# Optimization experiments

Measured on AMD Instinct MI355X. Metric: run time of the kernel, lower is better.

The kernel has to match this reference:

```python
import jax, jax.numpy as jnp
import numpy as np

B, S, D = 8, 1024, 1024          # batch, sentence_len, instance_size
H = 16                            # n_head
HEAD_SIZE = 1024                  # Head_size (== D here)
HD = HEAD_SIZE // H               # multi_head_size = 64


def setup_inputs() -> dict:
    key = jax.random.key(0)
    k1, k2, k3 = jax.random.split(key, 3)
    x = jax.random.normal(k1, (B, S, D), dtype=jnp.float32)
    padding_mask = jnp.ones((B, 1, S), dtype=jnp.float32)  # 1 = valid key token
    # nn.Linear(instance_size, 3*Head_size, bias=False): store as [D, 3*HEAD_SIZE]
    Wqkv = jax.random.normal(k2, (D, 3 * HEAD_SIZE), dtype=jnp.float32) / np.sqrt(D)
    # nn.Linear(Head_size, instance_size): weight [HEAD_SIZE, D] + bias [D]
    Wproj = jax.random.normal(k3, (HEAD_SIZE, D), dtype=jnp.float32) / np.sqrt(HEAD_SIZE)
    bproj = jnp.zeros((D,), dtype=jnp.float32)
    return {"x": x, "padding_mask": padding_mask, "Wqkv": Wqkv, "Wproj": Wproj, "bproj": bproj}


def reference(x, padding_mask, Wqkv, Wproj, bproj):
    Bn, Sn, _ = x.shape
    qkv = x @ Wqkv                                  # [B,S,3*HEAD_SIZE]
    q, k, v = jnp.split(qkv, 3, axis=2)
    # [B,S,H,hd] -> [B,H,S,hd]
    q = q.reshape(Bn, Sn, H, HD).transpose(0, 2, 1, 3)
    k = k.reshape(Bn, Sn, H, HD).transpose(0, 2, 1, 3)
    v = v.reshape(Bn, Sn, H, HD).transpose(0, 2, 1, 3)
    # scores [B,H,S,S]
    scores = jnp.einsum('bhqd,bhkd->bhqk', q, k) / np.sqrt(HD)
    # padding_mask [B,1,S] -> additive bias over key dim, broadcast over heads/queries
    mask_w = -(1.0 - padding_mask) * 1e10          # [B,1,S]
    scores = scores + mask_w[:, None]              # [B,1,1,S] broadcast
    probas = jax.nn.softmax(scores, axis=-1)
    probas = probas * padding_mask[:, None]        # zero out padded keys (as in torch code)
    # dropout p=0 (eval) -> identity
    out = jnp.einsum('bhqk,bhkd->bhqd', probas, v)  # [B,H,S,hd]
    out = out.transpose(0, 2, 1, 3).reshape(Bn, Sn, HEAD_SIZE)
    return out @ Wproj + bproj
```

## Files before the change

kernel.cpp:

```cpp
#include <hip/hip_runtime.h>
#include <stdint.h>

typedef short s16x8 __attribute__((ext_vector_type(8)));
typedef float f32x4 __attribute__((ext_vector_type(4)));
typedef unsigned short u16;
typedef unsigned short u16x4 __attribute__((ext_vector_type(4)));
typedef unsigned int u32x2 __attribute__((ext_vector_type(2)));

#define B_ 8
#define S_ 1024
#define C1 0.18033688f
#define KADV ((size_t)64 * 3072)

__device__ __forceinline__ u16 f2bf(float f) {
  union { float f; unsigned u; } v; v.f = f;
  unsigned u = v.u;
  unsigned r = (u + 0x7FFFu + ((u >> 16) & 1u)) >> 16;
  return (u16)r;
}

__device__ __forceinline__ void gll16(const u16* src, u16* dst) {
  __builtin_amdgcn_global_load_lds((const __attribute__((address_space(1))) void*)src,
                                   (__attribute__((address_space(3))) void*)dst, 16, 0, 0);
}

__global__ void k_cvt(const float* __restrict__ in, u16* __restrict__ out, int n4) {
  int i = blockIdx.x * blockDim.x + threadIdx.x;
  int stride = gridDim.x * blockDim.x;
  for (; i < n4; i += stride) {
    float4 v = ((const float4*)in)[i];
    u16x4 o;
    o.x = f2bf(v.x); o.y = f2bf(v.y); o.z = f2bf(v.z); o.w = f2bf(v.w);
    ((u16x4*)out)[i] = o;
  }
}

__global__ void k_mbias(const float* __restrict__ m, float* __restrict__ mb, int n) {
  int i = blockIdx.x * blockDim.x + threadIdx.x;
  if (i < n) mb[i] = (m[i] - 1.f) * 1.443e10f;
}

__global__ void k_tpose(const float* __restrict__ in, u16* __restrict__ out, int R, int C) {
  __shared__ float tile[64][65];
  int c0 = blockIdx.x * 64, r0 = blockIdx.y * 64;
  int t = threadIdx.x;
#pragma unroll
  for (int it = 0; it < 16; ++it) {
    int r = it * 4 + (t >> 6), c = t & 63;
    tile[r][c] = in[(size_t)(r0 + r) * C + c0 + c];
  }
  __syncthreads();
#pragma unroll
  for (int it = 0; it < 16; ++it) {
    int c = it * 4 + (t >> 6), r = t & 63;
    out[(size_t)(c0 + c) * R + r0 + r] = f2bf(tile[r][c]);
  }
}

template<int ROWS>
__device__ __forceinline__ void stage_swz(const u16* __restrict__ g, size_t goff, size_t ld,
                                          u16* lds, int wave, int lane) {
#pragma unroll
  for (int c = 0; c < ROWS / 32; ++c) {
    int jb = (wave * (ROWS / 32) + c) * 64;
    int j = jb + lane;
    int row = j >> 3;
    int s = (j & 7) ^ (row & 7);
    const u16* src = g + goff + (size_t)row * ld + s * 8;
    u16* dst = lds + jb * 8;
    gll16(src, dst);
  }
}

__device__ __forceinline__ s16x8 frag_read(const u16* lds, int row, int slotk) {
  int s = slotk ^ (row & 7);
  return *(const s16x8*)(lds + row * 64 + s * 8);
}

template<int BIAS, int OUT_F32, int QKV_VSPLIT>
__global__ __launch_bounds__(256, 2) void k_gemm(
    const u16* __restrict__ A, const u16* __restrict__ BT,
    void* __restrict__ Cout, const float* __restrict__ bias,
    int M, int N, int K) {
  __shared__ u16 sA[128 * 64];
  __shared__ u16 sB[128 * 64];
  int bid = blockIdx.x;
  int xcd = bid & 7, idx = bid >> 3;
  int tm = xcd * 8 + (idx & 7), tn = idx >> 3;
  int lane = threadIdx.x & 63, wave = threadIdx.x >> 6;
  int fr = lane & 15, g = lane >> 4;
  int wr = wave >> 1, wc = wave & 1;
  f32x4 acc[4][4] = {};
  for (int kt = 0; kt < (K >> 6); ++kt) {
    __syncthreads();
    stage_swz<128>(A, (size_t)(tm * 128) * K + kt * 64, K, sA, wave, lane);
    stage_swz<128>(BT, (size_t)(tn * 128) * K + kt * 64, K, sB, wave, lane);
    __syncthreads();
#pragma unroll
    for (int kk = 0; kk < 2; ++kk) {
      s16x8 af[4], bfr[4];
#pragma unroll
      for (int mi = 0; mi < 4; ++mi) af[mi] = frag_read(sA, wr * 64 + mi * 16 + fr, kk * 4 + g);
#pragma unroll
      for (int ni = 0; ni < 4; ++ni) bfr[ni] = frag_read(sB, wc * 64 + ni * 16 + fr, kk * 4 + g);
#pragma unroll
      for (int mi = 0; mi < 4; ++mi)
#pragma unroll
        for (int ni = 0; ni < 4; ++ni)
          acc[mi][ni] = __builtin_amdgcn_mfma_f32_16x16x32_bf16(af[mi], bfr[ni], acc[mi][ni], 0, 0, 0);
    }
  }
  if (QKV_VSPLIT && tn >= 16) {
#pragma unroll
    for (int mi = 0; mi < 4; ++mi) {
#pragma unroll
      for (int ni = 0; ni < 4; ++ni) {
        int row = tm * 128 + wr * 64 + mi * 16 + g * 4;
        int col = tn * 128 + wc * 64 + ni * 16 + fr;
        int colV = col - 2048;
        int rp = ((row >> 10) * 16 + (colV >> 6)) * 64 + (colV & 63);
        u16x4 o4;
#pragma unroll
        for (int r = 0; r < 4; ++r) o4[r] = f2bf(acc[mi][ni][r]);
        *(u16x4*)((u16*)Cout + (size_t)rp * 3072 + 2048 + (row & 1023)) = o4;
      }
    }
    return;
  }
#pragma unroll
  for (int mi = 0; mi < 4; ++mi) {
#pragma unroll
    for (int ni = 0; ni < 4; ++ni) {
      int row = tm * 128 + wr * 64 + mi * 16 + g * 4;
      int col = tn * 128 + wc * 64 + ni * 16 + fr;
      float bv = BIAS ? bias[col] : 0.f;
#pragma unroll
      for (int r = 0; r < 4; ++r) {
        float v = acc[mi][ni][r] + bv;
        if (OUT_F32) ((float*)Cout)[(size_t)(row + r) * N + col] = v;
        else ((u16*)Cout)[(size_t)(row + r) * N + col] = f2bf(v);
      }
    }
  }
}

__global__ __launch_bounds__(256, 4) void k_attn(
    const u16* __restrict__ qkv, const float* __restrict__ mbias, u16* __restrict__ outb) {
  __shared__ u16 kls[2][64 * 64];
  __shared__ u16 vls[2][64 * 64];
  int bid = blockIdx.x;
  int wg = (bid & 7) * 256 + (bid >> 3);
  int qt = wg & 15, h = (wg >> 4) & 15, b = wg >> 8;
  int lane = threadIdx.x & 63, wave = threadIdx.x >> 6;
  int fr = lane & 15, g = lane >> 4;

  const size_t baseK = (size_t)(b * S_) * 3072 + 1024 + h * 64;
  const size_t baseV = (size_t)((b * 16 + h) * 64) * 3072 + 2048;
  const float* mbc = mbias + b * S_ + g * 4;

  const size_t rowQ = (size_t)(b * S_ + qt * 64 + wave * 16 + fr) * 3072 + h * 64;
  s16x8 qf0 = *(const s16x8*)(qkv + rowQ + g * 8);
  s16x8 qf1 = *(const s16x8*)(qkv + rowQ + 32 + g * 8);

  int j0 = wave * 128 + lane, j1 = j0 + 64;
  int r0 = j0 >> 3, s0 = (j0 & 7) ^ (r0 & 7);
  int r1 = j1 >> 3, s1 = (j1 & 7) ^ (r1 & 7);
  const u16* kp0 = qkv + baseK + (size_t)r0 * 3072 + s0 * 8;
  const u16* kp1 = qkv + baseK + (size_t)r1 * 3072 + s1 * 8;
  const u16* vp0 = qkv + baseV + (size_t)r0 * 3072 + s0 * 8;
  const u16* vp1 = qkv + baseV + (size_t)r1 * 3072 + s1 * 8;
  u16* kd0 = (u16*)kls[0] + wave * 1024;
  u16* kd1 = kd0 + 512;
  u16* vd0 = (u16*)vls[0] + wave * 1024;
  u16* vd1 = vd0 + 512;

  const u16* kb = (const u16*)kls[0] + fr * 64;
  const u16* vb = (const u16*)vls[0] + fr * 64;
  const int sl0 = (g ^ (fr & 7)) * 8;
  const int sl4 = ((4 + g) ^ (fr & 7)) * 8;

  float se = 0.f;
  f32x4 oacc[4] = {};

  gll16(kp0, kd0); gll16(kp1, kd1); gll16(vp0, vd0); gll16(vp1, vd1);
  kp0 += KADV; kp1 += KADV; vp0 += 64; vp1 += 64;

#define CHUNK_BODY(BUF)                                                          \
  do {                                                                           \
    f32x4 b40 = *(const f32x4*)(mbc);                                            \
    f32x4 b41 = *(const f32x4*)(mbc + 16);                                       \
    f32x4 b42 = *(const f32x4*)(mbc + 32);                                       \
    f32x4 b43 = *(const f32x4*)(mbc + 48);                                       \
    unsigned wv[4][2];                                                           \
    float ss0 = 0.f, ss1 = 0.f, ss2 = 0.f, ss3 = 0.f;                            \
    _Pragma("unroll") for (int kt = 0; kt < 4; ++kt) {                           \
      f32x4 sacc = {0.f, 0.f, 0.f, 0.f};                                         \
      s16x8 kf0 = *(const s16x8*)(kb + (BUF)*4096 + kt * 1024 + sl0);            \
      s16x8 kf1 = *(const s16x8*)(kb + (BUF)*4096 + kt * 1024 + sl4);            \
      sacc = __builtin_amdgcn_mfma_f32_16x16x32_bf16(kf0, qf0, sacc, 0, 0, 0);   \
      sacc = __builtin_amdgcn_mfma_f32_16x16x32_bf16(kf1, qf1, sacc, 0, 0, 0);   \
      f32x4 b4 = (kt == 0) ? b40 : (kt == 1) ? b41 : (kt == 2) ? b42 : b43;      \
      float e0 = exp2f(fmaf(sacc[0], C1, b4[0]));                                \
      float e1 = exp2f(fmaf(sacc[1], C1, b4[1]));                                \
      float e2 = exp2f(fmaf(sacc[2], C1, b4[2]));                                \
      float e3 = exp2f(fmaf(sacc[3], C1, b4[3]));                                \
      ss0 += e0; ss1 += e1; ss2 += e2; ss3 += e3;                                \
      asm("v_cvt_pk_bf16_f32 %0, %1, %2" : "=v"(wv[kt][0]) : "v"(e0), "v"(e1));  \
      asm("v_cvt_pk_bf16_f32 %0, %1, %2" : "=v"(wv[kt][1]) : "v"(e2), "v"(e3));  \
    }                                                                            \
    se += (ss0 + ss1) + (ss2 + ss3);                                             \
    _Pragma("unroll") for (int kc = 0; kc < 2; ++kc) {                           \
      unsigned x0 = wv[2 * kc][0], y0 = wv[2 * kc + 1][0];                       \
      unsigned x1 = wv[2 * kc][1], y1 = wv[2 * kc + 1][1];                       \
      asm("v_permlane32_swap_b32 %0, %1" : "+v"(x0), "+v"(y0));                  \
      asm("v_permlane16_swap_b32 %0, %1" : "+v"(x0), "+v"(y0));                  \
      asm("v_permlane32_swap_b32 %0, %1" : "+v"(x1), "+v"(y1));                  \
      asm("v_permlane16_swap_b32 %0, %1" : "+v"(x1), "+v"(y1));                  \
      union { unsigned u[4]; s16x8 v; } pfu;                                     \
      pfu.u[0] = x0; pfu.u[1] = x1; pfu.u[2] = y0; pfu.u[3] = y1;                \
      _Pragma("unroll") for (int dbi = 0; dbi < 4; ++dbi) {                      \
        s16x8 vf = *(const s16x8*)(vb + (BUF)*4096 + dbi * 1024 +                \
                                   ((kc) ? sl4 : sl0));                          \
        oacc[dbi] = __builtin_amdgcn_mfma_f32_16x16x32_bf16(vf, pfu.v,           \
                                                            oacc[dbi], 0, 0, 0); \
      }                                                                          \
    }                                                                            \
    mbc += 64;                                                                   \
  } while (0)

#pragma unroll 1
  for (int chp = 0; chp < 8; ++chp) {
    __syncthreads();
    gll16(kp0, kd0 + 4096); gll16(kp1, kd1 + 4096);
    gll16(vp0, vd0 + 4096); gll16(vp1, vd1 + 4096);
    kp0 += KADV; kp1 += KADV; vp0 += 64; vp1 += 64;
    CHUNK_BODY(0);
    __syncthreads();
    if (chp < 7) {
      gll16(kp0, kd0); gll16(kp1, kd1); gll16(vp0, vd0); gll16(vp1, vd1);
      kp0 += KADV; kp1 += KADV; vp0 += 64; vp1 += 64;
    }
    CHUNK_BODY(1);
  }
#undef CHUNK_BODY

  se += __shfl_xor(se, 16);
  se += __shfl_xor(se, 32);
  float inv = 1.f / se;
  u16* orow = outb + (size_t)(b * S_ + qt * 64 + wave * 16 + fr) * 1024 + h * 64;
#pragma unroll
  for (int dbi = 0; dbi < 4; ++dbi) {
    float o0 = oacc[dbi][0] * inv, o1 = oacc[dbi][1] * inv;
    float o2 = oacc[dbi][2] * inv, o3 = oacc[dbi][3] * inv;
    unsigned w0, w1;
    asm("v_cvt_pk_bf16_f32 %0, %1, %2" : "=v"(w0) : "v"(o0), "v"(o1));
    asm("v_cvt_pk_bf16_f32 %0, %1, %2" : "=v"(w1) : "v"(o2), "v"(o3));
    u32x2 ww = {w0, w1};
    *(u32x2*)(orow + dbi * 16 + g * 4) = ww;
  }
}

extern "C" void kernel_launch(void* const* d_in, const int* in_sizes, int n_in,
                              void* d_out, int out_size, void* d_ws, size_t ws_size,
                              hipStream_t stream) {
  const float* x     = (const float*)d_in[0];
  const float* pmask = (const float*)d_in[1];
  const float* Wqkv  = (const float*)d_in[2];
  const float* Wproj = (const float*)d_in[3];
  const float* bproj = (const float*)d_in[4];

  u16* xB      = (u16*)d_ws;
  u16* WqkvT   = xB + (size_t)8192 * 1024;
  u16* WprojT  = WqkvT + (size_t)3072 * 1024;
  u16* qkv     = WprojT + (size_t)1024 * 1024;
  u16* attn    = qkv + (size_t)8192 * 3072;
  float* mbias = (float*)(attn + (size_t)8192 * 1024);

  k_cvt<<<2048, 256, 0, stream>>>(x, xB, 8192 * 1024 / 4);
  k_mbias<<<32, 256, 0, stream>>>(pmask, mbias, 8192);
  k_tpose<<<dim3(3072 / 64, 1024 / 64), 256, 0, stream>>>(Wqkv, WqkvT, 1024, 3072);
  k_tpose<<<dim3(1024 / 64, 1024 / 64), 256, 0, stream>>>(Wproj, WprojT, 1024, 1024);
  k_gemm<0, 0, 1><<<64 * 24, 256, 0, stream>>>(xB, WqkvT, (void*)qkv, (const float*)nullptr, 8192, 3072, 1024);
  k_attn<<<2048, 256, 0, stream>>>(qkv, mbias, attn);
  k_gemm<1, 1, 0><<<64 * 8, 256, 0, stream>>>(attn, WprojT, d_out, bproj, 8192, 1024, 1024);
}
```

Measured before the change: 169.0 us.

## Process 128 queries per attention block to reuse K/V tiles across two query groups

```diff
diff --git a/kernel.cpp b/kernel.cpp
--- a/kernel.cpp
+++ b/kernel.cpp
@@ -149,8 +149,8 @@
   __shared__ u16 kls[2][64 * 64];
   __shared__ u16 vls[2][64 * 64];
   int bid = blockIdx.x;
-  int wg = (bid & 7) * 256 + (bid >> 3);
-  int qt = wg & 15, h = (wg >> 4) & 15, b = wg >> 8;
+  int wg = (bid & 7) * 128 + (bid >> 3);
+  int qt = wg & 7, h = (wg >> 3) & 15, b = wg >> 7;
   int lane = threadIdx.x & 63, wave = threadIdx.x >> 6;
   int fr = lane & 15, g = lane >> 4;
 
@@ -158,9 +158,12 @@
   const size_t baseV = (size_t)((b * 16 + h) * 64) * 3072 + 2048;
   const float* mbc = mbias + b * S_ + g * 4;
 
-  const size_t rowQ = (size_t)(b * S_ + qt * 64 + wave * 16 + fr) * 3072 + h * 64;
-  s16x8 qf0 = *(const s16x8*)(qkv + rowQ + g * 8);
-  s16x8 qf1 = *(const s16x8*)(qkv + rowQ + 32 + g * 8);
+  const size_t rowQA = (size_t)(b * S_ + qt * 128 + wave * 32 + fr) * 3072 + h * 64;
+  const size_t rowQB = rowQA + (size_t)16 * 3072;
+  s16x8 qfA0 = *(const s16x8*)(qkv + rowQA + g * 8);
+  s16x8 qfA1 = *(const s16x8*)(qkv + rowQA + 32 + g * 8);
+  s16x8 qfB0 = *(const s16x8*)(qkv + rowQB + g * 8);
+  s16x8 qfB1 = *(const s16x8*)(qkv + rowQB + 32 + g * 8);
 
   int j0 = wave * 128 + lane, j1 = j0 + 64;
   int r0 = j0 >> 3, s0 = (j0 & 7) ^ (r0 & 7);
@@ -179,8 +182,9 @@
   const int sl0 = (g ^ (fr & 7)) * 8;
   const int sl4 = ((4 + g) ^ (fr & 7)) * 8;
 
-  float se = 0.f;
-  f32x4 oacc[4] = {};
+  float seA = 0.f, seB = 0.f;
+  f32x4 oaccA[4] = {};
+  f32x4 oaccB[4] = {};
 
   gll16(kp0, kd0); gll16(kp1, kd1); gll16(vp0, vd0); gll16(vp1, vd1);
   kp0 += KADV; kp1 += KADV; vp0 += 64; vp1 += 64;
@@ -191,38 +195,58 @@
     f32x4 b41 = *(const f32x4*)(mbc + 16);                                       \
     f32x4 b42 = *(const f32x4*)(mbc + 32);                                       \
     f32x4 b43 = *(const f32x4*)(mbc + 48);                                       \
-    unsigned wv[4][2];                                                           \
-    float ss0 = 0.f, ss1 = 0.f, ss2 = 0.f, ss3 = 0.f;                            \
+    unsigned wvA[4][2], wvB[4][2];                                               \
+    float sA0 = 0.f, sA1 = 0.f, sA2 = 0.f, sA3 = 0.f;                            \
+    float sB0 = 0.f, sB1 = 0.f, sB2 = 0.f, sB3 = 0.f;                            \
     _Pragma("unroll") for (int kt = 0; kt < 4; ++kt) {                           \
-      f32x4 sacc = {0.f, 0.f, 0.f, 0.f};                                         \
       s16x8 kf0 = *(const s16x8*)(kb + (BUF)*4096 + kt * 1024 + sl0);            \
       s16x8 kf1 = *(const s16x8*)(kb + (BUF)*4096 + kt * 1024 + sl4);            \
-      sacc = __builtin_amdgcn_mfma_f32_16x16x32_bf16(kf0, qf0, sacc, 0, 0, 0);   \
-      sacc = __builtin_amdgcn_mfma_f32_16x16x32_bf16(kf1, qf1, sacc, 0, 0, 0);   \
+      f32x4 sa = {0.f, 0.f, 0.f, 0.f}, sb = {0.f, 0.f, 0.f, 0.f};                \
+      sa = __builtin_amdgcn_mfma_f32_16x16x32_bf16(kf0, qfA0, sa, 0, 0, 0);      \
+      sa = __builtin_amdgcn_mfma_f32_16x16x32_bf16(kf1, qfA1, sa, 0, 0, 0);      \
+      sb = __builtin_amdgcn_mfma_f32_16x16x32_bf16(kf0, qfB0, sb, 0, 0, 0);      \
+      sb = __builtin_amdgcn_mfma_f32_16x16x32_bf16(kf1, qfB1, sb, 0, 0, 0);      \
       f32x4 b4 = (kt == 0) ? b40 : (kt == 1) ? b41 : (kt == 2) ? b42 : b43;      \
-      float e0 = exp2f(fmaf(sacc[0], C1, b4[0]));                                \
-      float e1 = exp2f(fmaf(sacc[1], C1, b4[1]));                                \
-      float e2 = exp2f(fmaf(sacc[2], C1, b4[2]));                                \
-      float e3 = exp2f(fmaf(sacc[3], C1, b4[3]));                                \
-      ss0 += e0; ss1 += e1; ss2 += e2; ss3 += e3;                                \
-      asm("v_cvt_pk_bf16_f32 %0, %1, %2" : "=v"(wv[kt][0]) : "v"(e0), "v"(e1));  \
-      asm("v_cvt_pk_bf16_f32 %0, %1, %2" : "=v"(wv[kt][1]) : "v"(e2), "v"(e3));  \
+      float eA0 = exp2f(fmaf(sa[0], C1, b4[0]));                                 \
+      float eA1 = exp2f(fmaf(sa[1], C1, b4[1]));                                 \
+      float eA2 = exp2f(fmaf(sa[2], C1, b4[2]));                                 \
+      float eA3 = exp2f(fmaf(sa[3], C1, b4[3]));                                 \
+      float eB0 = exp2f(fmaf(sb[0], C1, b4[0]));                                 \
+      float eB1 = exp2f(fmaf(sb[1], C1, b4[1]));                                 \
+      float eB2 = exp2f(fmaf(sb[2], C1, b4[2]));                                 \
+      float eB3 = exp2f(fmaf(sb[3], C1, b4[3]));                                 \
+      sA0 += eA0; sA1 += eA1; sA2 += eA2; sA3 += eA3;                            \
+      sB0 += eB0; sB1 += eB1; sB2 += eB2; sB3 += eB3;                            \
+      asm("v_cvt_pk_bf16_f32 %0, %1, %2" : "=v"(wvA[kt][0]) : "v"(eA0), "v"(eA1)); \
+      asm("v_cvt_pk_bf16_f32 %0, %1, %2" : "=v"(wvA[kt][1]) : "v"(eA2), "v"(eA3)); \
+      asm("v_cvt_pk_bf16_f32 %0, %1, %2" : "=v"(wvB[kt][0]) : "v"(eB0), "v"(eB1)); \
+      asm("v_cvt_pk_bf16_f32 %0, %1, %2" : "=v"(wvB[kt][1]) : "v"(eB2), "v"(eB3)); \
     }                                                                            \
-    se += (ss0 + ss1) + (ss2 + ss3);                                             \
+    seA += (sA0 + sA1) + (sA2 + sA3);                                            \
+    seB += (sB0 + sB1) + (sB2 + sB3);                                            \
     _Pragma("unroll") for (int kc = 0; kc < 2; ++kc) {                           \
-      unsigned x0 = wv[2 * kc][0], y0 = wv[2 * kc + 1][0];                       \
-      unsigned x1 = wv[2 * kc][1], y1 = wv[2 * kc + 1][1];                       \
-      asm("v_permlane32_swap_b32 %0, %1" : "+v"(x0), "+v"(y0));                  \
-      asm("v_permlane16_swap_b32 %0, %1" : "+v"(x0), "+v"(y0));                  \
-      asm("v_permlane32_swap_b32 %0, %1" : "+v"(x1), "+v"(y1));                  \
-      asm("v_permlane16_swap_b32 %0, %1" : "+v"(x1), "+v"(y1));                  \
-      union { unsigned u[4]; s16x8 v; } pfu;                                     \
-      pfu.u[0] = x0; pfu.u[1] = x1; pfu.u[2] = y0; pfu.u[3] = y1;                \
+      unsigned xa0 = wvA[2 * kc][0], ya0 = wvA[2 * kc + 1][0];                   \
+      unsigned xa1 = wvA[2 * kc][1], ya1 = wvA[2 * kc + 1][1];                   \
+      unsigned xb0 = wvB[2 * kc][0], yb0 = wvB[2 * kc + 1][0];                   \
+      unsigned xb1 = wvB[2 * kc][1], yb1 = wvB[2 * kc + 1][1];                   \
+      asm("v_permlane32_swap_b32 %0, %1" : "+v"(xa0), "+v"(ya0));                \
+      asm("v_permlane16_swap_b32 %0, %1" : "+v"(xa0), "+v"(ya0));                \
+      asm("v_permlane32_swap_b32 %0, %1" : "+v"(xa1), "+v"(ya1));                \
+      asm("v_permlane16_swap_b32 %0, %1" : "+v"(xa1), "+v"(ya1));                \
+      asm("v_permlane32_swap_b32 %0, %1" : "+v"(xb0), "+v"(yb0));                \
+      asm("v_permlane16_swap_b32 %0, %1" : "+v"(xb0), "+v"(yb0));                \
+      asm("v_permlane32_swap_b32 %0, %1" : "+v"(xb1), "+v"(yb1));                \
+      asm("v_permlane16_swap_b32 %0, %1" : "+v"(xb1), "+v"(yb1));                \
+      union { unsigned u[4]; s16x8 v; } pfa, pfb;                                \
+      pfa.u[0] = xa0; pfa.u[1] = xa1; pfa.u[2] = ya0; pfa.u[3] = ya1;            \
+      pfb.u[0] = xb0; pfb.u[1] = xb1; pfb.u[2] = yb0; pfb.u[3] = yb1;            \
       _Pragma("unroll") for (int dbi = 0; dbi < 4; ++dbi) {                      \
         s16x8 vf = *(const s16x8*)(vb + (BUF)*4096 + dbi * 1024 +                \
                                    ((kc) ? sl4 : sl0));                          \
-        oacc[dbi] = __builtin_amdgcn_mfma_f32_16x16x32_bf16(vf, pfu.v,           \
-                                                            oacc[dbi], 0, 0, 0); \
+        oaccA[dbi] = __builtin_amdgcn_mfma_f32_16x16x32_bf16(vf, pfa.v,          \
+                                                             oaccA[dbi], 0, 0, 0); \
+        oaccB[dbi] = __builtin_amdgcn_mfma_f32_16x16x32_bf16(vf, pfb.v,          \
+                                                             oaccB[dbi], 0, 0, 0); \
       }                                                                          \
     }                                                                            \
     mbc += 64;                                                                   \
@@ -244,19 +268,27 @@
   }
 #undef CHUNK_BODY
 
-  se += __shfl_xor(se, 16);
-  se += __shfl_xor(se, 32);
-  float inv = 1.f / se;
-  u16* orow = outb + (size_t)(b * S_ + qt * 64 + wave * 16 + fr) * 1024 + h * 64;
+  seA += __shfl_xor(seA, 16);
+  seA += __shfl_xor(seA, 32);
+  seB += __shfl_xor(seB, 16);
+  seB += __shfl_xor(seB, 32);
+  float invA = 1.f / seA, invB = 1.f / seB;
+  u16* orowA = outb + (size_t)(b * S_ + qt * 128 + wave * 32 + fr) * 1024 + h * 64;
+  u16* orowB = orowA + (size_t)16 * 1024;
 #pragma unroll
   for (int dbi = 0; dbi < 4; ++dbi) {
-    float o0 = oacc[dbi][0] * inv, o1 = oacc[dbi][1] * inv;
-    float o2 = oacc[dbi][2] * inv, o3 = oacc[dbi][3] * inv;
-    unsigned w0, w1;
-    asm("v_cvt_pk_bf16_f32 %0, %1, %2" : "=v"(w0) : "v"(o0), "v"(o1));
-    asm("v_cvt_pk_bf16_f32 %0, %1, %2" : "=v"(w1) : "v"(o2), "v"(o3));
-    u32x2 ww = {w0, w1};
-    *(u32x2*)(orow + dbi * 16 + g * 4) = ww;
+    float a0 = oaccA[dbi][0] * invA, a1 = oaccA[dbi][1] * invA;
+    float a2 = oaccA[dbi][2] * invA, a3 = oaccA[dbi][3] * invA;
+    float b0 = oaccB[dbi][0] * invB, b1 = oaccB[dbi][1] * invB;
+    float b2 = oaccB[dbi][2] * invB, b3 = oaccB[dbi][3] * invB;
+    unsigned wa0, wa1, wb0, wb1;
+    asm("v_cvt_pk_bf16_f32 %0, %1, %2" : "=v"(wa0) : "v"(a0), "v"(a1));
+    asm("v_cvt_pk_bf16_f32 %0, %1, %2" : "=v"(wa1) : "v"(a2), "v"(a3));
+    asm("v_cvt_pk_bf16_f32 %0, %1, %2" : "=v"(wb0) : "v"(b0), "v"(b1));
+    asm("v_cvt_pk_bf16_f32 %0, %1, %2" : "=v"(wb1) : "v"(b2), "v"(b3));
+    u32x2 wwa = {wa0, wa1}, wwb = {wb0, wb1};
+    *(u32x2*)(orowA + dbi * 16 + g * 4) = wwa;
+    *(u32x2*)(orowB + dbi * 16 + g * 4) = wwb;
   }
 }
 
@@ -281,6 +313,6 @@
   k_tpose<<<dim3(3072 / 64, 1024 / 64), 256, 0, stream>>>(Wqkv, WqkvT, 1024, 3072);
   k_tpose<<<dim3(1024 / 64, 1024 / 64), 256, 0, stream>>>(Wproj, WprojT, 1024, 1024);
   k_gemm<0, 0, 1><<<64 * 24, 256, 0, stream>>>(xB, WqkvT, (void*)qkv, (const float*)nullptr, 8192, 3072, 1024);
-  k_attn<<<2048, 256, 0, stream>>>(qkv, mbias, attn);
+  k_attn<<<1024, 256, 0, stream>>>(qkv, mbias, attn);
   k_gemm<1, 1, 0><<<64 * 8, 256, 0, stream>>>(attn, WprojT, d_out, bproj, 8192, 1024, 1024);
 }
```

After: 168.1 us. No clear change (-0.6%).
